# Kernel optimization log

Hardware: AMD Instinct MI355X
Metric: run time of the kernel (lower is better)

Reference implementation:

```python
import jax, jax.numpy as jnp
import numpy as np

N_NODES = 100000
N_EDGES = 3200000
STATE_DIM = 128
ACTION_DIM = 8


def _w(key, shape, scale=0.05):
    return (jax.random.normal(key, shape, dtype=jnp.float32) * scale)


def setup_inputs() -> dict:
    key = jax.random.key(0)
    ks = jax.random.split(key, 24)
    x = jax.random.normal(ks[0], (N_NODES, STATE_DIM), dtype=jnp.float32)
    edge_index = jax.random.randint(ks[1], (2, N_EDGES), 0, N_NODES, dtype=jnp.int64)
    inp = {
        "x": x,
        "edge_index": edge_index,
        # GCN layers (weights stored [in, out] so forward is x @ W + b)
        "W1": _w(ks[2], (STATE_DIM, 128)), "b1": jnp.zeros((128,), jnp.float32),
        "W2": _w(ks[3], (128, 128)),       "b2": jnp.zeros((128,), jnp.float32),
        "W3": _w(ks[4], (128, 64)),        "b3": jnp.zeros((64,), jnp.float32),
        # actor MLP 64->128->64->ACTION_DIM + softmax
        "Wa1": _w(ks[5], (64, 128)),  "ba1": jnp.zeros((128,), jnp.float32),
        "Wa2": _w(ks[6], (128, 64)),  "ba2": jnp.zeros((64,), jnp.float32),
        "Wa3": _w(ks[7], (64, ACTION_DIM)), "ba3": jnp.zeros((ACTION_DIM,), jnp.float32),
        # critic MLP 64->128->64->1
        "Wc1": _w(ks[8], (64, 128)),  "bc1": jnp.zeros((128,), jnp.float32),
        "Wc2": _w(ks[9], (128, 64)),  "bc2": jnp.zeros((64,), jnp.float32),
        "Wc3": _w(ks[10], (64, 1)),   "bc3": jnp.zeros((1,), jnp.float32),
    }
    return inp


def _gcn_conv(x, W, b, src, dst, norm):
    # GCNConv: D^{-1/2} (A + I) D^{-1/2} X W + b  (self loops already in src/dst)
    h = x @ W                                   # [N, out]
    msg = h[src] * norm[:, None]                # gather + per-edge scale
    agg = jax.ops.segment_sum(msg, dst, num_segments=N_NODES)
    return agg + b


def reference(x, edge_index,
              W1, b1, W2, b2, W3, b3,
              Wa1, ba1, Wa2, ba2, Wa3, ba3,
              Wc1, bc1, Wc2, bc2, Wc3, bc3):
    loop = jnp.arange(N_NODES, dtype=edge_index.dtype)
    src = jnp.concatenate([edge_index[0], loop])
    dst = jnp.concatenate([edge_index[1], loop])
    deg = jax.ops.segment_sum(jnp.ones_like(dst, dtype=x.dtype), dst,
                              num_segments=N_NODES)
    dinv = jax.lax.rsqrt(deg)                   # deg >= 1 via self loops
    norm = dinv[src] * dinv[dst]                # [E+N]

    # forward_gnn (dropout is identity in eval mode)
    h = jax.nn.relu(_gcn_conv(x, W1, b1, src, dst, norm))
    h = jax.nn.relu(_gcn_conv(h, W2, b2, src, dst, norm))
    h = _gcn_conv(h, W3, b3, src, dst, norm)    # [N, 64]

    a = jax.nn.relu(h @ Wa1 + ba1)
    a = jax.nn.relu(a @ Wa2 + ba2)
    probs = jax.nn.softmax(a @ Wa3 + ba3, axis=-1)   # [N, ACTION_DIM]

    c = jax.nn.relu(h @ Wc1 + bc1)
    c = jax.nn.relu(c @ Wc2 + bc2)
    values = c @ Wc3 + bc3                      # [N, 1]

    return jnp.concatenate([probs, values], axis=-1)  # [N, ACTION_DIM+1]
```

## Files before the change

kernel.cpp:

```cpp
#include <hip/hip_runtime.h>
#include <hip/hip_bf16.h>
#include <math.h>


#define WS_ALIGN(x) (((x) + 255) & ~(size_t)255)

constexpr int RNG  = 64;
constexpr int NRG  = 1563;
constexpr int NB   = 1024;
constexpr int CHK  = 16;

constexpr float S_FP8     = 64.0f;
constexpr float S_FP8_INV = 1.0f / 64.0f;

using bf16x8 = __attribute__((ext_vector_type(8))) short;
using f32x4  = __attribute__((ext_vector_type(4))) float;
using f32x2  = __attribute__((ext_vector_type(2))) float;

__device__ __forceinline__ float b2f(unsigned short u) {
    return __uint_as_float(((unsigned int)u) << 16);
}
__device__ __forceinline__ unsigned short f2b(float f) {
    __hip_bfloat16 hb = __float2bfloat16(f);
    return *(unsigned short*)&hb;
}
__device__ __forceinline__ unsigned char f2fp8(float f) {
    return (unsigned char)(__builtin_amdgcn_cvt_pk_fp8_f32(f, f, 0, false) & 0xff);
}
__device__ __forceinline__ int pad8(int v) { return (v + 7) & ~7; }

__device__ __forceinline__ void acc8(uint2 u, f32x2& a01, f32x2& a23,
                                     f32x2& a45, f32x2& a67) {
    a01 += __builtin_amdgcn_cvt_pk_f32_fp8((int)u.x, false);
    a23 += __builtin_amdgcn_cvt_pk_f32_fp8((int)u.x, true);
    a45 += __builtin_amdgcn_cvt_pk_f32_fp8((int)u.y, false);
    a67 += __builtin_amdgcn_cvt_pk_f32_fp8((int)u.y, true);
}


__global__ __launch_bounds__(256) void bucket_count_k(
    const int* __restrict__ dst, int* __restrict__ bcnt, int E,
    const float* __restrict__ W1, const float* __restrict__ W2,
    const float* __restrict__ W3, const float* __restrict__ Wa1,
    const float* __restrict__ Wc1, const float* __restrict__ Wa2,
    const float* __restrict__ Wc2,
    const float* __restrict__ b1, const float* __restrict__ b2,
    const float* __restrict__ b3,
    unsigned short* __restrict__ wt, float* __restrict__ bp) {
    __shared__ int c64[RNG];
    int b = blockIdx.x, t = threadIdx.x;

    int gi = b * 256 + t;
    if (gi < 73728) {
        const float* W; int off, K, OUT; int pm = 0;
        if (gi < 16384)      { W = W1;  off = 0;     K = 128; OUT = 128; }
        else if (gi < 32768) { W = W2;  off = 16384; K = 128; OUT = 128; pm = 1; }
        else if (gi < 40960) { W = W3;  off = 32768; K = 128; OUT = 64;  pm = 1; }
        else if (gi < 49152) { W = Wa1; off = 40960; K = 64;  OUT = 128; pm = 2; }
        else if (gi < 57344) { W = Wc1; off = 49152; K = 64;  OUT = 128; pm = 2; }
        else if (gi < 65536) { W = Wa2; off = 57344; K = 128; OUT = 64; }
        else                 { W = Wc2; off = 65536; K = 128; OUT = 64; }
        int j = gi - off, k = j / OUT, n = j - k * OUT;
        int kp = (pm == 1) ? ((k & 15) * 8 + (k >> 4))
               : (pm == 2) ? ((k & 15) * 4 + (k >> 4)) : k;
        wt[off + n * K + kp] = f2b(W[j]);
    } else if (gi < 74048) {
        int j = gi - 73728;
        if (j < 128)      bp[(j & 15) * 8 + (j >> 4)] = b1[j];
        else if (j < 256) { int j2 = j - 128; bp[128 + (j2 & 15) * 8 + (j2 >> 4)] = b2[j2]; }
        else              { int j3 = j - 256; bp[256 + (j3 & 15) * 4 + (j3 >> 4)] = b3[j3]; }
    }

    if (t < RNG) c64[t] = 0;
    __syncthreads();
    int ec = (E + NB - 1) / NB;
    int e0 = b * ec, e1 = min(E, e0 + ec);
    for (int e = e0 + t; e < e1; e += 256) {
        int d = __builtin_nontemporal_load(dst + e);
        atomicAdd(&c64[d / NRG], 1);
    }
    __syncthreads();
    if (t < RNG) bcnt[t * NB + b] = c64[t];
}

__global__ __launch_bounds__(256) void rsum_k(
    const int* __restrict__ bcnt, int* __restrict__ base, int* __restrict__ rtot) {
    __shared__ int s[256];
    int r = blockIdx.x, t = threadIdx.x;
    const int* row = bcnt + (size_t)r * NB;
    int v[4], loc = 0;
#pragma unroll
    for (int j = 0; j < 4; j++) { v[j] = row[t * 4 + j]; loc += v[j]; }
    s[t] = loc;
    __syncthreads();
    for (int d = 1; d < 256; d <<= 1) {
        int x = (t >= d) ? s[t - d] : 0;
        __syncthreads();
        s[t] += x;
        __syncthreads();
    }
    int run = s[t] - loc;
    int* bp2 = base + (size_t)r * NB + t * 4;
#pragma unroll
    for (int j = 0; j < 4; j++) { bp2[j] = run; run += v[j]; }
    if (t == 255) rtot[r] = s[255];
}

__global__ __launch_bounds__(256) void bucket_scatter_k(
    const int* __restrict__ src, const int* __restrict__ dst,
    const int* __restrict__ base, const int* __restrict__ rtot,
    unsigned* __restrict__ bucket, int E) {
    __shared__ int cur[RNG];
    __shared__ int rt[RNG];
    int b = blockIdx.x, t = threadIdx.x;
    if (t < RNG) rt[t] = rtot[t];
    __syncthreads();
    if (t < RNG) {
        int run = 0;
        for (int j = 0; j < t; j++) run += rt[j];
        cur[t] = run + base[(size_t)t * NB + b];
    }
    __syncthreads();
    int ec = (E + NB - 1) / NB;
    int e0 = b * ec, e1 = min(E, e0 + ec);
    for (int e = e0 + t; e < e1; e += 256) {
        int d = __builtin_nontemporal_load(dst + e);
        int sv = __builtin_nontemporal_load(src + e);
        int r = d / NRG;
        int pos = atomicAdd(&cur[r], 1);
        bucket[pos] = ((unsigned)(d - r * NRG) << 17) | (unsigned)sv;
    }
}

__global__ __launch_bounds__(256) void hist_bucket_k(
    const unsigned* __restrict__ bucket, const int* __restrict__ rtot,
    int* __restrict__ hist) {
    __shared__ int h[NRG];
    __shared__ int ss[2];
    int b = blockIdx.x, r = b & 63, c2 = b >> 6, t = threadIdx.x;
    for (int i = t; i < NRG; i += 256) h[i] = 0;
    if (t == 0) {
        int run = 0;
        for (int j = 0; j < r; j++) run += rtot[j];
        ss[0] = run; ss[1] = run + rtot[r];
    }
    __syncthreads();
    int s0 = ss[0], s1 = ss[1];
    int ec = (s1 - s0 + CHK - 1) / CHK;
    int e0 = s0 + c2 * ec, e1 = min(s1, e0 + ec);
    for (int e = e0 + t; e < e1; e += 256) {
        unsigned v = __builtin_nontemporal_load(bucket + e);
        atomicAdd(&h[v >> 17], 1);
    }
    __syncthreads();
    int* out = hist + ((size_t)r * CHK + c2) * NRG;
    for (int i = t; i < NRG; i += 256) out[i] = h[i];
}

__global__ __launch_bounds__(256) void sum_hist_dinv_k(
    const int* __restrict__ hist, int* __restrict__ cnt,
    float* __restrict__ dinv, int* __restrict__ bsum, int N) {
    __shared__ int sd[256];
    int t = threadIdx.x;
    int i = blockIdx.x * 256 + t;
    int s = 0;
    if (i < N) {
        int r = i / NRG, li = i - r * NRG;
        const int* hp = hist + ((size_t)r * CHK) * NRG + li;
#pragma unroll
        for (int c = 0; c < CHK; c++) s += hp[(size_t)c * NRG];
        cnt[i] = s;
        dinv[i] = rsqrtf((float)s + 1.0f);
    }
    sd[t] = (i < N) ? pad8(s) : 0;
    __syncthreads();
    for (int d = 128; d > 0; d >>= 1) {
        if (t < d) sd[t] += sd[t + d];
        __syncthreads();
    }
    if (t == 0) bsum[blockIdx.x] = sd[0];
}

__global__ void scan_off_pad_k(const int* __restrict__ cnt, const int* __restrict__ bsum,
                               int* __restrict__ rowptr, int* __restrict__ hist,
                               int* __restrict__ col, int N) {
    __shared__ int s[256];
    int t = threadIdx.x, b = blockIdx.x;

    int part = 0;
    for (int j = t; j < b; j += 256) part += bsum[j];
    s[t] = part;
    __syncthreads();
    for (int d = 128; d > 0; d >>= 1) {
        if (t < d) s[t] += s[t + d];
        __syncthreads();
    }
    int boffv = s[0];
    __syncthreads();

    int i = b * 256 + t;
    int cv = (i < N) ? cnt[i] : 0;
    int v = pad8(cv);
    if (i >= N) v = 0;
    s[t] = v;
    __syncthreads();
    for (int d = 1; d < 256; d <<= 1) {
        int x = (t >= d) ? s[t - d] : 0;
        __syncthreads();
        s[t] += x;
        __syncthreads();
    }
    if (b == (int)gridDim.x - 1 && t == 255) rowptr[N] = boffv + s[255];
    if (i < N) {
        int rp = s[t] - v + boffv;
        rowptr[i] = rp;
        int r = i / NRG, li = i - r * NRG;
        int* hp = hist + ((size_t)r * CHK) * NRG + li;
        int run = rp;
#pragma unroll
        for (int c = 0; c < CHK; c++) {
            int hv = hp[(size_t)c * NRG];
            hp[(size_t)c * NRG] = run;
            run += hv;
        }
        for (int e = rp + cv; e < rp + v; e++) col[e] = N;
    }
}

__global__ __launch_bounds__(256) void fill2_k(
    const unsigned* __restrict__ bucket, const int* __restrict__ rtot,
    const int* __restrict__ hist, int* __restrict__ col) {
    __shared__ int cur[NRG];
    __shared__ int ss[2];
    int b = blockIdx.x, r = b & 63, c2 = b >> 6, t = threadIdx.x;
    const int* hp = hist + ((size_t)r * CHK + c2) * NRG;
    for (int i = t; i < NRG; i += 256) cur[i] = hp[i];
    if (t == 0) {
        int run = 0;
        for (int j = 0; j < r; j++) run += rtot[j];
        ss[0] = run; ss[1] = run + rtot[r];
    }
    __syncthreads();
    int s0 = ss[0], s1 = ss[1];
    int ec = (s1 - s0 + CHK - 1) / CHK;
    int e0 = s0 + c2 * ec, e1 = min(s1, e0 + ec);
    for (int e = e0 + t; e < e1; e += 256) {
        unsigned v = __builtin_nontemporal_load(bucket + e);
        int slot = atomicAdd(&cur[v >> 17], 1);
        col[slot] = (int)(v & 0x1FFFFu);
    }
}


template <int K, int OUT, int EPI, bool AF32>
__global__ __launch_bounds__(256) void gemm2_k(
    const void* __restrict__ Xv, int ldx, const unsigned short* __restrict__ Wt,
    const float* __restrict__ sb, const float* __restrict__ w3b,
    const float* __restrict__ b3, void* __restrict__ Yv, int N, int NT) {
    constexpr int LDK = K + 8;
    __shared__ __align__(16) unsigned short Bs[OUT * LDK];
    __shared__ __align__(16) unsigned short As[64 * LDK];
    int t = threadIdx.x;

    for (int g = t; g < OUT * (K / 8); g += 256) {
        int r = g / (K / 8), q = g - r * (K / 8);
        *(uint4*)&Bs[r * LDK + q * 8] = *(const uint4*)(Wt + r * K + q * 8);
    }

    int wv = t >> 6, lane = t & 63;
    int lm = lane & 15, lq = lane >> 4;
    constexpr int CT = OUT / 16;

    for (int tile = blockIdx.x; tile < NT; tile += gridDim.x) {
        int rowBase = tile * 64;

        if constexpr (AF32) {
            const float* X = (const float*)Xv;
            for (int g = t; g < 64 * (K / 8); g += 256) {
                int r = g / (K / 8), q = g - r * (K / 8);
                int gr = rowBase + r;
                unsigned short us[8];
                if (gr < N) {
                    float4 v0 = *(const float4*)(X + (size_t)gr * ldx + q * 8);
                    float4 v1 = *(const float4*)(X + (size_t)gr * ldx + q * 8 + 4);
                    us[0] = f2b(v0.x); us[1] = f2b(v0.y); us[2] = f2b(v0.z); us[3] = f2b(v0.w);
                    us[4] = f2b(v1.x); us[5] = f2b(v1.y); us[6] = f2b(v1.z); us[7] = f2b(v1.w);
                } else {
#pragma unroll
                    for (int j = 0; j < 8; j++) us[j] = 0;
                }
                *(uint4*)&As[r * LDK + q * 8] = *(uint4*)us;
            }
        } else {
            const unsigned short* X = (const unsigned short*)Xv;
            for (int g = t; g < 64 * (K / 8); g += 256) {
                int r = g / (K / 8), q = g - r * (K / 8);
                int gr = rowBase + r;
                uint4 v = make_uint4(0, 0, 0, 0);
                if (gr < N) v = *(const uint4*)(X + (size_t)gr * ldx + q * 8);
                *(uint4*)&As[r * LDK + q * 8] = v;
            }
        }
        __syncthreads();

        f32x4 acc[CT];
#pragma unroll
        for (int c = 0; c < CT; c++) acc[c] = (f32x4){0.f, 0.f, 0.f, 0.f};

        const unsigned short* arow = &As[(wv * 16 + lm) * LDK + lq * 8];
#pragma unroll
        for (int kt = 0; kt < K / 32; kt++) {
            bf16x8 a = *(const bf16x8*)(arow + kt * 32);
#pragma unroll
            for (int c = 0; c < CT; c++) {
                bf16x8 b = *(const bf16x8*)&Bs[(c * 16 + lm) * LDK + kt * 32 + lq * 8];
                acc[c] = __builtin_amdgcn_mfma_f32_16x16x32_bf16(a, b, acc[c], 0, 0, 0);
            }
        }

        int r0 = rowBase + wv * 16 + lq * 4;
        if constexpr (EPI == 0) {
#pragma unroll
            for (int r = 0; r < 4; r++) {
                int gr = r0 + r;
                float scale = (gr < N) ? sb[gr] * S_FP8 : 0.f;
                if constexpr (OUT == 128) {
                    unsigned w0 = 0, w1 = 0;
                    w0 = __builtin_amdgcn_cvt_pk_fp8_f32(acc[0][r] * scale, acc[1][r] * scale, w0, false);
                    w0 = __builtin_amdgcn_cvt_pk_fp8_f32(acc[2][r] * scale, acc[3][r] * scale, w0, true);
                    w1 = __builtin_amdgcn_cvt_pk_fp8_f32(acc[4][r] * scale, acc[5][r] * scale, w1, false);
                    w1 = __builtin_amdgcn_cvt_pk_fp8_f32(acc[6][r] * scale, acc[7][r] * scale, w1, true);
                    *(uint2*)((unsigned char*)Yv + (size_t)gr * 128 + lm * 8) = make_uint2(w0, w1);
                } else {
                    unsigned w0 = 0;
                    w0 = __builtin_amdgcn_cvt_pk_fp8_f32(acc[0][r] * scale, acc[1][r] * scale, w0, false);
                    w0 = __builtin_amdgcn_cvt_pk_fp8_f32(acc[2][r] * scale, acc[3][r] * scale, w0, true);
                    *(unsigned*)((unsigned char*)Yv + (size_t)gr * 64 + lm * 4) = w0;
                }
            }
        }
        __syncthreads();
    }
}


template <bool RELU>
__global__ __launch_bounds__(256) void agg128_k(
    const unsigned char* __restrict__ H,
    const int* __restrict__ rowptr, const int* __restrict__ col,
    const float* __restrict__ dinv, const float* __restrict__ bias,
    unsigned short* __restrict__ Y, int N, int Ecap) {
    int tid = threadIdx.x;
    int node = blockIdx.x * 4 + (tid >> 6);
    if (node >= N) return;
    int lane = tid & 63;
    int grp = lane >> 4;
    int li8 = (lane & 15) * 8;

    f32x2 a01 = {0.f, 0.f}, a23 = {0.f, 0.f}, a45 = {0.f, 0.f}, a67 = {0.f, 0.f};
    if (grp == 0) {
        uint2 u = *(const uint2*)(H + (size_t)node * 128 + li8);
        acc8(u, a01, a23, a45, a67);
    }

    int start = rowptr[node], end = rowptr[node + 1];
    for (int e0 = start; e0 < end; e0 += 64) {
        int cv = col[min(e0 + lane, Ecap - 1)];
        int quads = min(64, end - e0) >> 2;
        for (int q = 0; q < quads; q += 2) {
            int s0 = __shfl(cv, 4 * q + grp, 64);
            int s1 = __shfl(cv, 4 * q + 4 + grp, 64);
            uint2 u0 = *(const uint2*)(H + (size_t)s0 * 128 + li8);
            uint2 u1 = *(const uint2*)(H + (size_t)s1 * 128 + li8);
            acc8(u0, a01, a23, a45, a67);
            acc8(u1, a01, a23, a45, a67);
        }
    }

#pragma unroll
    for (int w = 16; w < 64; w <<= 1) {
        a01[0] += __shfl_xor(a01[0], w, 64); a01[1] += __shfl_xor(a01[1], w, 64);
        a23[0] += __shfl_xor(a23[0], w, 64); a23[1] += __shfl_xor(a23[1], w, 64);
        a45[0] += __shfl_xor(a45[0], w, 64); a45[1] += __shfl_xor(a45[1], w, 64);
        a67[0] += __shfl_xor(a67[0], w, 64); a67[1] += __shfl_xor(a67[1], w, 64);
    }

    if (grp == 0) {
        float dv = dinv[node] * S_FP8_INV;
        float4 b0 = *(const float4*)(bias + li8);
        float4 b1 = *(const float4*)(bias + li8 + 4);
        float o0 = a01[0] * dv + b0.x, o1 = a01[1] * dv + b0.y;
        float o2 = a23[0] * dv + b0.z, o3 = a23[1] * dv + b0.w;
        float o4 = a45[0] * dv + b1.x, o5 = a45[1] * dv + b1.y;
        float o6 = a67[0] * dv + b1.z, o7 = a67[1] * dv + b1.w;
        if (RELU) {
            o0 = fmaxf(o0, 0.f); o1 = fmaxf(o1, 0.f); o2 = fmaxf(o2, 0.f); o3 = fmaxf(o3, 0.f);
            o4 = fmaxf(o4, 0.f); o5 = fmaxf(o5, 0.f); o6 = fmaxf(o6, 0.f); o7 = fmaxf(o7, 0.f);
        }
        unsigned short us[8] = {f2b(o0), f2b(o1), f2b(o2), f2b(o3),
                                f2b(o4), f2b(o5), f2b(o6), f2b(o7)};
        *(uint4*)(Y + (size_t)node * 128 + li8) = *(uint4*)us;
    }
}

__global__ __launch_bounds__(256) void agg64_k(
    const unsigned char* __restrict__ H,
    const int* __restrict__ rowptr, const int* __restrict__ col,
    const float* __restrict__ dinv, const float* __restrict__ bias,
    unsigned short* __restrict__ Y, int N, int Ecap) {
    int tid = threadIdx.x;
    int node = blockIdx.x * 4 + (tid >> 6);
    if (node >= N) return;
    int lane = tid & 63;
    int grp = lane >> 3;
    int li8 = (lane & 7) * 8;

    f32x2 a01 = {0.f, 0.f}, a23 = {0.f, 0.f}, a45 = {0.f, 0.f}, a67 = {0.f, 0.f};
    if (grp == 0) {
        uint2 u = *(const uint2*)(H + (size_t)node * 64 + li8);
        acc8(u, a01, a23, a45, a67);
    }

    int start = rowptr[node], end = rowptr[node + 1];
    for (int e0 = start; e0 < end; e0 += 64) {
        int cv = col[min(e0 + lane, Ecap - 1)];
        int octs = min(64, end - e0) >> 3;
        int o = 0;
        for (; o + 2 <= octs; o += 2) {
            int s0 = __shfl(cv, 8 * o + grp, 64);
            int s1 = __shfl(cv, 8 * o + 8 + grp, 64);
            uint2 u0 = *(const uint2*)(H + (size_t)s0 * 64 + li8);
            uint2 u1 = *(const uint2*)(H + (size_t)s1 * 64 + li8);
            acc8(u0, a01, a23, a45, a67);
            acc8(u1, a01, a23, a45, a67);
        }
        if (o < octs) {
            int s0 = __shfl(cv, 8 * o + grp, 64);
            uint2 u0 = *(const uint2*)(H + (size_t)s0 * 64 + li8);
            acc8(u0, a01, a23, a45, a67);
        }
    }

#pragma unroll
    for (int w = 8; w < 64; w <<= 1) {
        a01[0] += __shfl_xor(a01[0], w, 64); a01[1] += __shfl_xor(a01[1], w, 64);
        a23[0] += __shfl_xor(a23[0], w, 64); a23[1] += __shfl_xor(a23[1], w, 64);
        a45[0] += __shfl_xor(a45[0], w, 64); a45[1] += __shfl_xor(a45[1], w, 64);
        a67[0] += __shfl_xor(a67[0], w, 64); a67[1] += __shfl_xor(a67[1], w, 64);
    }

    if (grp == 0) {
        float dv = dinv[node] * S_FP8_INV;
        float4 b0 = *(const float4*)(bias + li8);
        float4 b1 = *(const float4*)(bias + li8 + 4);
        unsigned short us[8] = {
            f2b(a01[0] * dv + b0.x), f2b(a01[1] * dv + b0.y),
            f2b(a23[0] * dv + b0.z), f2b(a23[1] * dv + b0.w),
            f2b(a45[0] * dv + b1.x), f2b(a45[1] * dv + b1.y),
            f2b(a67[0] * dv + b1.z), f2b(a67[1] * dv + b1.w)};
        *(uint4*)(Y + (size_t)node * 64 + li8) = *(uint4*)us;
    }
}


__global__ __launch_bounds__(256) void headsB_k(
    const unsigned short* __restrict__ h3,
    const unsigned short* __restrict__ Wh1t,
    const float* __restrict__ ba1, const float* __restrict__ bc1,
    const unsigned short* __restrict__ Wa2t,
    const float* __restrict__ ba2,
    const unsigned short* __restrict__ Wc2t,
    const float* __restrict__ bc2,
    const float* __restrict__ Wa3, const float* __restrict__ ba3,
    const float* __restrict__ Wc3, const float* __restrict__ bc3,
    float* __restrict__ out, int N, int NT, int GH) {
    constexpr int LD64 = 72, LD128 = 136;
    __shared__ __align__(16) unsigned short Bs1[128 * LD64];
    __shared__ __align__(16) unsigned short Bs2[64 * LD128];
    __shared__ __align__(16) unsigned short As[4 * 16 * LD64];
    __shared__ __align__(16) unsigned short A1[4 * 16 * LD128];
    int t = threadIdx.x, wv = t >> 6, lane = t & 63;
    int lm = lane & 15, lq = lane >> 4;

    bool actor = (int)blockIdx.x < GH;
    const unsigned short* W1t = actor ? Wh1t : Wh1t + 128 * 64;
    const float* b1v = actor ? ba1 : bc1;
    const unsigned short* W2t = actor ? Wa2t : Wc2t;
    const float* b2v = actor ? ba2 : bc2;
    const float* w3  = actor ? Wa3 : Wc3;
    const float* b3v = actor ? ba3 : bc3;
    int tile0 = actor ? (int)blockIdx.x : (int)blockIdx.x - GH;

    for (int g = t; g < 128 * 8; g += 256) {
        int r = g >> 3, q = g & 7;
        *(uint4*)&Bs1[r * LD64 + q * 8] = *(const uint4*)(W1t + r * 64 + q * 8);
    }
    for (int g = t; g < 64 * 16; g += 256) {
        int r = g >> 4, q = g & 15;
        *(uint4*)&Bs2[r * LD128 + q * 8] = *(const uint4*)(W2t + r * 128 + q * 8);
    }
    __syncthreads();

    unsigned short* Asw = &As[wv * 16 * LD64];
    unsigned short* A1w = &A1[wv * 16 * LD128];

    for (int tile = tile0; tile < NT; tile += GH) {
        int rowBase = tile * 64 + wv * 16;

        for (int g = lane; g < 16 * 8; g += 64) {
            int r = g >> 3, q = g & 7;
            int gr = rowBase + r;
            uint4 v = make_uint4(0, 0, 0, 0);
            if (gr < N) v = *(const uint4*)(h3 + (size_t)gr * 64 + q * 8);
            *(uint4*)&Asw[r * LD64 + q * 8] = v;
        }

        f32x4 acc1[8];
#pragma unroll
        for (int c = 0; c < 8; c++) acc1[c] = (f32x4){0.f, 0.f, 0.f, 0.f};
        const unsigned short* arow = &Asw[lm * LD64 + lq * 8];
#pragma unroll
        for (int kt = 0; kt < 2; kt++) {
            bf16x8 a = *(const bf16x8*)(arow + kt * 32);
#pragma unroll
            for (int c = 0; c < 8; c++) {
                bf16x8 b = *(const bf16x8*)&Bs1[(c * 16 + lm) * LD64 + kt * 32 + lq * 8];
                acc1[c] = __builtin_amdgcn_mfma_f32_16x16x32_bf16(a, b, acc1[c], 0, 0, 0);
            }
        }
#pragma unroll
        for (int r = 0; r < 4; r++) {
            int lr = lq * 4 + r;
#pragma unroll
            for (int c = 0; c < 8; c++) {
                int colg = c * 16 + lm;
                float v = fmaxf(acc1[c][r] + b1v[colg], 0.f);
                A1w[lr * LD128 + colg] = f2b(v);
            }
        }

        f32x4 acc[4];
#pragma unroll
        for (int c = 0; c < 4; c++) acc[c] = (f32x4){0.f, 0.f, 0.f, 0.f};
        const unsigned short* arow2 = &A1w[lm * LD128 + lq * 8];
#pragma unroll
        for (int kt = 0; kt < 4; kt++) {
            bf16x8 a = *(const bf16x8*)(arow2 + kt * 32);
#pragma unroll
            for (int c = 0; c < 4; c++) {
                bf16x8 b = *(const bf16x8*)&Bs2[(c * 16 + lm) * LD128 + kt * 32 + lq * 8];
                acc[c] = __builtin_amdgcn_mfma_f32_16x16x32_bf16(a, b, acc[c], 0, 0, 0);
            }
        }

        int r0 = rowBase + lq * 4;
        if (actor) {
            float l[4][8];
#pragma unroll
            for (int r = 0; r < 4; r++)
#pragma unroll
                for (int a = 0; a < 8; a++) l[r][a] = 0.f;
#pragma unroll
            for (int c = 0; c < 4; c++) {
                int colg = c * 16 + lm;
#pragma unroll
                for (int r = 0; r < 4; r++) {
                    float v = fmaxf(acc[c][r] + b2v[colg], 0.f);
#pragma unroll
                    for (int a = 0; a < 8; a++)
                        l[r][a] = fmaf(v, w3[colg * 8 + a], l[r][a]);
                }
            }
#pragma unroll
            for (int w = 1; w < 16; w <<= 1)
#pragma unroll
                for (int r = 0; r < 4; r++)
#pragma unroll
                    for (int a = 0; a < 8; a++)
                        l[r][a] += __shfl_xor(l[r][a], w, 64);
            if (lm < 8) {
#pragma unroll
                for (int r = 0; r < 4; r++) {
                    int gr = r0 + r;
                    if (gr < N) {
                        float lg[8], m = -1e30f;
#pragma unroll
                        for (int a = 0; a < 8; a++) { lg[a] = l[r][a] + b3v[a]; m = fmaxf(m, lg[a]); }
                        float sum = 0.f;
#pragma unroll
                        for (int a = 0; a < 8; a++) { lg[a] = expf(lg[a] - m); sum += lg[a]; }
                        out[(size_t)gr * 9 + lm] = lg[lm] / sum;
                    }
                }
            }
        } else {
            float lv[4] = {0.f, 0.f, 0.f, 0.f};
#pragma unroll
            for (int c = 0; c < 4; c++) {
                int colg = c * 16 + lm;
#pragma unroll
                for (int r = 0; r < 4; r++) {
                    float v = fmaxf(acc[c][r] + b2v[colg], 0.f);
                    lv[r] = fmaf(v, w3[colg], lv[r]);
                }
            }
#pragma unroll
            for (int w = 1; w < 16; w <<= 1)
#pragma unroll
                for (int r = 0; r < 4; r++) lv[r] += __shfl_xor(lv[r], w, 64);
            if (lm == 0) {
#pragma unroll
                for (int r = 0; r < 4; r++) {
                    int gr = r0 + r;
                    if (gr < N) out[(size_t)gr * 9 + 8] = lv[r] + b3v[0];
                }
            }
        }
    }
}


extern "C" void kernel_launch(void* const* d_in, const int* in_sizes, int n_in,
                              void* d_out, int out_size, void* d_ws, size_t ws_size,
                              hipStream_t stream) {
    const float* x   = (const float*)d_in[0];
    const int*   ei  = (const int*)d_in[1];
    const float* W1  = (const float*)d_in[2];  const float* b1  = (const float*)d_in[3];
    const float* W2  = (const float*)d_in[4];  const float* b2  = (const float*)d_in[5];
    const float* W3  = (const float*)d_in[6];  const float* b3  = (const float*)d_in[7];
    const float* Wa1 = (const float*)d_in[8];  const float* ba1 = (const float*)d_in[9];
    const float* Wa2 = (const float*)d_in[10]; const float* ba2 = (const float*)d_in[11];
    const float* Wa3 = (const float*)d_in[12]; const float* ba3 = (const float*)d_in[13];
    const float* Wc1 = (const float*)d_in[14]; const float* bc1 = (const float*)d_in[15];
    const float* Wc2 = (const float*)d_in[16]; const float* bc2 = (const float*)d_in[17];
    const float* Wc3 = (const float*)d_in[18]; const float* bc3 = (const float*)d_in[19];
    float* out = (float*)d_out;

    const int N = in_sizes[0] / 128;
    const int E = in_sizes[1] / 2;
    const int* src = ei;
    const int* dst = ei + E;
    const int Ecap = E + 8 * N;
    const int Npad = ((N + 63) / 64) * 64;
    const int NT   = (N + 63) / 64;

    size_t off = 0;
    auto take = [&](size_t bytes) { size_t o = off; off = WS_ALIGN(off + bytes); return o; };
    char* ws = (char*)d_ws;
    unsigned short* h3     = (unsigned short*)(ws + take((size_t)N * 64 * 2));
    unsigned short* h      = (unsigned short*)(ws + take((size_t)N * 128 * 2));
    unsigned char*  hpr8   = (unsigned char*) (ws + take((size_t)(Npad + 64) * 128));
    int*            col    = (int*)(ws + take((size_t)Ecap * 4));
    unsigned short* wt     = (unsigned short*)(ws + take(73728 * 2));
    float* bperm  = (float*)(ws + take(320 * 4));
    float* dinv   = (float*)(ws + take((size_t)(N + 64) * 4));
    int*   cnt    = (int*)  (ws + take((size_t)N * 4));
    int*   rowptr = (int*)  (ws + take((size_t)(N + 1) * 4));
    int*   bcnt   = (int*)  (ws + take((size_t)RNG * NB * 4));
    int*   base   = (int*)  (ws + take((size_t)RNG * NB * 4));
    int*   rtot   = (int*)  (ws + take(RNG * 4));
    int*   bsum   = (int*)  (ws + take(512 * 4));
    unsigned* bucket = (unsigned*)h;
    int* hist = (int*)h3;
    (void)ws_size; (void)n_in; (void)out_size;

    const int nb  = (N + 255) / 256;
    const int GG128 = 768;
    const int GG64  = 1024;
    const int GH    = 512;

    const unsigned short* W1t  = wt;
    const unsigned short* W2t  = wt + 16384;
    const unsigned short* W3t  = wt + 32768;
    const unsigned short* Wh1t = wt + 40960;
    const unsigned short* Wa2t = wt + 57344;
    const unsigned short* Wc2t = wt + 65536;
    const float* b1p = bperm;
    const float* b2p = bperm + 128;
    const float* b3p = bperm + 256;

    bucket_count_k<<<NB, 256, 0, stream>>>(dst, bcnt, E,
                                           W1, W2, W3, Wa1, Wc1, Wa2, Wc2,
                                           b1, b2, b3, wt, bperm);
    rsum_k<<<RNG, 256, 0, stream>>>(bcnt, base, rtot);
    bucket_scatter_k<<<NB, 256, 0, stream>>>(src, dst, base, rtot, bucket, E);
    hist_bucket_k<<<RNG * CHK, 256, 0, stream>>>(bucket, rtot, hist);
    sum_hist_dinv_k<<<nb, 256, 0, stream>>>(hist, cnt, dinv, bsum, N);
    scan_off_pad_k<<<nb, 256, 0, stream>>>(cnt, bsum, rowptr, hist, col, N);
    fill2_k<<<RNG * CHK, 256, 0, stream>>>(bucket, rtot, hist, col);

    gemm2_k<128, 128, 0, true><<<GG128, 256, 0, stream>>>(
        x, 128, W1t, dinv, nullptr, nullptr, hpr8, N, NT);
    agg128_k<true><<<(N + 3) / 4, 256, 0, stream>>>(hpr8, rowptr, col, dinv, b1p, h, N, Ecap);
    gemm2_k<128, 128, 0, false><<<GG128, 256, 0, stream>>>(
        h, 128, W2t, dinv, nullptr, nullptr, hpr8, N, NT);
    agg128_k<true><<<(N + 3) / 4, 256, 0, stream>>>(hpr8, rowptr, col, dinv, b2p, h, N, Ecap);
    gemm2_k<128, 64, 0, false><<<GG64, 256, 0, stream>>>(
        h, 128, W3t, dinv, nullptr, nullptr, hpr8, N, NT);
    agg64_k<<<(N + 3) / 4, 256, 0, stream>>>(hpr8, rowptr, col, dinv, b3p, h3, N, Ecap);

    headsB_k<<<2 * GH, 256, 0, stream>>>(
        h3, Wh1t, ba1, bc1, Wa2t, ba2, Wc2t, bc2, Wa3, ba3, Wc3, bc3, out, N, NT, GH);
}
```

Measured before the change: 458.9 us.

## Fold histogram into bucket scatter and co-schedule CSR fill with first GEMM

The per-chunk destination histogram is now built with global atomics inside the bucket scatter kernel, which removes the separate hist_bucket pass over the bucket array. The hist buffer is zeroed in the first kernel. The CSR column fill and the layer-1 GEMM are merged into one launch, with blocks split 4:3 by block index, so these two independent tasks can overlap on the GPU. In exchange, 3.2M global atomics replace shared-memory atomics, and the fused kernel's shared footprint is sized for the GEMM, which may lower occupancy for the fill blocks.

```diff
diff --git a/kernel.cpp b/kernel.cpp
--- a/kernel.cpp
+++ b/kernel.cpp
@@ -9,6 +9,7 @@
 constexpr int NRG  = 1563;
 constexpr int NB   = 1024;
 constexpr int CHK  = 16;
+constexpr int HISTN = RNG * CHK * NRG;
 
 constexpr float S_FP8     = 64.0f;
 constexpr float S_FP8_INV = 1.0f / 64.0f;
@@ -46,7 +47,8 @@
     const float* __restrict__ Wc2,
     const float* __restrict__ b1, const float* __restrict__ b2,
     const float* __restrict__ b3,
-    unsigned short* __restrict__ wt, float* __restrict__ bp) {
+    unsigned short* __restrict__ wt, float* __restrict__ bp,
+    int* __restrict__ hist) {
     __shared__ int c64[RNG];
     int b = blockIdx.x, t = threadIdx.x;
 
@@ -71,6 +73,8 @@
         else              { int j3 = j - 256; bp[256 + (j3 & 15) * 4 + (j3 >> 4)] = b3[j3]; }
     }
 
+    for (int i2 = gi; i2 < HISTN; i2 += NB * 256) hist[i2] = 0;
+
     if (t < RNG) c64[t] = 0;
     __syncthreads();
     int ec = (E + NB - 1) / NB;
@@ -109,8 +113,10 @@
 __global__ __launch_bounds__(256) void bucket_scatter_k(
     const int* __restrict__ src, const int* __restrict__ dst,
     const int* __restrict__ base, const int* __restrict__ rtot,
-    unsigned* __restrict__ bucket, int E) {
+    unsigned* __restrict__ bucket, int* __restrict__ hist, int E) {
     __shared__ int cur[RNG];
+    __shared__ int sstart[RNG];
+    __shared__ int ecs[RNG];
     __shared__ int rt[RNG];
     int b = blockIdx.x, t = threadIdx.x;
     if (t < RNG) rt[t] = rtot[t];
@@ -118,7 +124,9 @@
     if (t < RNG) {
         int run = 0;
         for (int j = 0; j < t; j++) run += rt[j];
+        sstart[t] = run;
         cur[t] = run + base[(size_t)t * NB + b];
+        ecs[t] = (rt[t] + CHK - 1) / CHK;
     }
     __syncthreads();
     int ec = (E + NB - 1) / NB;
@@ -126,35 +134,12 @@
     for (int e = e0 + t; e < e1; e += 256) {
         int d = __builtin_nontemporal_load(dst + e);
         int sv = __builtin_nontemporal_load(src + e);
-        int r = d / NRG;
+        int r = d / NRG, li = d - r * NRG;
         int pos = atomicAdd(&cur[r], 1);
-        bucket[pos] = ((unsigned)(d - r * NRG) << 17) | (unsigned)sv;
-    }
-}
-
-__global__ __launch_bounds__(256) void hist_bucket_k(
-    const unsigned* __restrict__ bucket, const int* __restrict__ rtot,
-    int* __restrict__ hist) {
-    __shared__ int h[NRG];
-    __shared__ int ss[2];
-    int b = blockIdx.x, r = b & 63, c2 = b >> 6, t = threadIdx.x;
-    for (int i = t; i < NRG; i += 256) h[i] = 0;
-    if (t == 0) {
-        int run = 0;
-        for (int j = 0; j < r; j++) run += rtot[j];
-        ss[0] = run; ss[1] = run + rtot[r];
-    }
-    __syncthreads();
-    int s0 = ss[0], s1 = ss[1];
-    int ec = (s1 - s0 + CHK - 1) / CHK;
-    int e0 = s0 + c2 * ec, e1 = min(s1, e0 + ec);
-    for (int e = e0 + t; e < e1; e += 256) {
-        unsigned v = __builtin_nontemporal_load(bucket + e);
-        atomicAdd(&h[v >> 17], 1);
-    }
-    __syncthreads();
-    int* out = hist + ((size_t)r * CHK + c2) * NRG;
-    for (int i = t; i < NRG; i += 256) out[i] = h[i];
+        bucket[pos] = ((unsigned)li << 17) | (unsigned)sv;
+        int c2 = (int)((unsigned)(pos - sstart[r]) / (unsigned)ecs[r]);
+        atomicAdd(&hist[((size_t)r * CHK + c2) * NRG + li], 1);
+    }
 }
 
 __global__ __launch_bounds__(256) void sum_hist_dinv_k(
@@ -227,27 +212,97 @@
     }
 }
 
-__global__ __launch_bounds__(256) void fill2_k(
+
+__global__ __launch_bounds__(256) void fill2_gemm1_k(
     const unsigned* __restrict__ bucket, const int* __restrict__ rtot,
-    const int* __restrict__ hist, int* __restrict__ col) {
-    __shared__ int cur[NRG];
-    __shared__ int ss[2];
-    int b = blockIdx.x, r = b & 63, c2 = b >> 6, t = threadIdx.x;
-    const int* hp = hist + ((size_t)r * CHK + c2) * NRG;
-    for (int i = t; i < NRG; i += 256) cur[i] = hp[i];
-    if (t == 0) {
-        int run = 0;
-        for (int j = 0; j < r; j++) run += rtot[j];
-        ss[0] = run; ss[1] = run + rtot[r];
-    }
-    __syncthreads();
-    int s0 = ss[0], s1 = ss[1];
-    int ec = (s1 - s0 + CHK - 1) / CHK;
-    int e0 = s0 + c2 * ec, e1 = min(s1, e0 + ec);
-    for (int e = e0 + t; e < e1; e += 256) {
-        unsigned v = __builtin_nontemporal_load(bucket + e);
-        int slot = atomicAdd(&cur[v >> 17], 1);
-        col[slot] = (int)(v & 0x1FFFFu);
+    const int* __restrict__ hist, int* __restrict__ col,
+    const float* __restrict__ X, const unsigned short* __restrict__ Wt,
+    const float* __restrict__ dinv, unsigned char* __restrict__ Y,
+    int N, int NT) {
+    constexpr int LDK = 136;
+    __shared__ __align__(16) unsigned char smem[(128 * LDK + 64 * LDK) * 2];
+    int bid = blockIdx.x, t = threadIdx.x;
+    int sel = bid % 7;
+
+    if (sel < 4) {
+        int b = (bid / 7) * 4 + sel;
+        int* cur = (int*)smem;
+        int* ss  = (int*)(smem + NRG * 4);
+        int r = b & 63, c2 = b >> 6;
+        const int* hp = hist + ((size_t)r * CHK + c2) * NRG;
+        for (int i = t; i < NRG; i += 256) cur[i] = hp[i];
+        if (t == 0) {
+            int run = 0;
+            for (int j = 0; j < r; j++) run += rtot[j];
+            ss[0] = run; ss[1] = run + rtot[r];
+        }
+        __syncthreads();
+        int s0 = ss[0], s1 = ss[1];
+        int ec = (s1 - s0 + CHK - 1) / CHK;
+        int e0 = s0 + c2 * ec, e1 = min(s1, e0 + ec);
+        for (int e = e0 + t; e < e1; e += 256) {
+            unsigned v = __builtin_nontemporal_load(bucket + e);
+            int slot = atomicAdd(&cur[v >> 17], 1);
+            col[slot] = (int)(v & 0x1FFFFu);
+        }
+    } else {
+        int gb = (bid / 7) * 3 + (sel - 4);
+        unsigned short* Bs = (unsigned short*)smem;
+        unsigned short* As = (unsigned short*)(smem + 128 * LDK * 2);
+        for (int g = t; g < 128 * 16; g += 256) {
+            int r = g >> 4, q = g & 15;
+            *(uint4*)&Bs[r * LDK + q * 8] = *(const uint4*)(Wt + r * 128 + q * 8);
+        }
+        int wv = t >> 6, lane = t & 63;
+        int lm = lane & 15, lq = lane >> 4;
+
+        for (int tile = gb; tile < NT; tile += 768) {
+            int rowBase = tile * 64;
+            for (int g = t; g < 64 * 16; g += 256) {
+                int r = g >> 4, q = g & 15;
+                int gr = rowBase + r;
+                unsigned short us[8];
+                if (gr < N) {
+                    float4 v0 = *(const float4*)(X + (size_t)gr * 128 + q * 8);
+                    float4 v1 = *(const float4*)(X + (size_t)gr * 128 + q * 8 + 4);
+                    us[0] = f2b(v0.x); us[1] = f2b(v0.y); us[2] = f2b(v0.z); us[3] = f2b(v0.w);
+                    us[4] = f2b(v1.x); us[5] = f2b(v1.y); us[6] = f2b(v1.z); us[7] = f2b(v1.w);
+                } else {
+#pragma unroll
+                    for (int j = 0; j < 8; j++) us[j] = 0;
+                }
+                *(uint4*)&As[r * LDK + q * 8] = *(uint4*)us;
+            }
+            __syncthreads();
+
+            f32x4 acc[8];
+#pragma unroll
+            for (int c = 0; c < 8; c++) acc[c] = (f32x4){0.f, 0.f, 0.f, 0.f};
+            const unsigned short* arow = &As[(wv * 16 + lm) * LDK + lq * 8];
+#pragma unroll
+            for (int kt = 0; kt < 4; kt++) {
+                bf16x8 a = *(const bf16x8*)(arow + kt * 32);
+#pragma unroll
+                for (int c = 0; c < 8; c++) {
+                    bf16x8 bfrag = *(const bf16x8*)&Bs[(c * 16 + lm) * LDK + kt * 32 + lq * 8];
+                    acc[c] = __builtin_amdgcn_mfma_f32_16x16x32_bf16(a, bfrag, acc[c], 0, 0, 0);
+                }
+            }
+
+            int r0 = rowBase + wv * 16 + lq * 4;
+#pragma unroll
+            for (int r = 0; r < 4; r++) {
+                int gr = r0 + r;
+                float scale = (gr < N) ? dinv[gr] * S_FP8 : 0.f;
+                unsigned w0 = 0, w1 = 0;
+                w0 = __builtin_amdgcn_cvt_pk_fp8_f32(acc[0][r] * scale, acc[1][r] * scale, w0, false);
+                w0 = __builtin_amdgcn_cvt_pk_fp8_f32(acc[2][r] * scale, acc[3][r] * scale, w0, true);
+                w1 = __builtin_amdgcn_cvt_pk_fp8_f32(acc[4][r] * scale, acc[5][r] * scale, w1, false);
+                w1 = __builtin_amdgcn_cvt_pk_fp8_f32(acc[6][r] * scale, acc[7][r] * scale, w1, true);
+                *(uint2*)(Y + (size_t)gr * 128 + lm * 8) = make_uint2(w0, w1);
+            }
+            __syncthreads();
+        }
     }
 }
 
@@ -681,16 +736,15 @@
 
     bucket_count_k<<<NB, 256, 0, stream>>>(dst, bcnt, E,
                                            W1, W2, W3, Wa1, Wc1, Wa2, Wc2,
-                                           b1, b2, b3, wt, bperm);
+                                           b1, b2, b3, wt, bperm, hist);
     rsum_k<<<RNG, 256, 0, stream>>>(bcnt, base, rtot);
-    bucket_scatter_k<<<NB, 256, 0, stream>>>(src, dst, base, rtot, bucket, E);
-    hist_bucket_k<<<RNG * CHK, 256, 0, stream>>>(bucket, rtot, hist);
+    bucket_scatter_k<<<NB, 256, 0, stream>>>(src, dst, base, rtot, bucket, hist, E);
     sum_hist_dinv_k<<<nb, 256, 0, stream>>>(hist, cnt, dinv, bsum, N);
     scan_off_pad_k<<<nb, 256, 0, stream>>>(cnt, bsum, rowptr, hist, col, N);
-    fill2_k<<<RNG * CHK, 256, 0, stream>>>(bucket, rtot, hist, col);
-
-    gemm2_k<128, 128, 0, true><<<GG128, 256, 0, stream>>>(
-        x, 128, W1t, dinv, nullptr, nullptr, hpr8, N, NT);
+
+    fill2_gemm1_k<<<1792, 256, 0, stream>>>(bucket, rtot, hist, col,
+                                            x, W1t, dinv, hpr8, N, NT);
+
     agg128_k<true><<<(N + 3) / 4, 256, 0, stream>>>(hpr8, rowptr, col, dinv, b1p, h, N, Ecap);
     gemm2_k<128, 128, 0, false><<<GG128, 256, 0, stream>>>(
         h, 128, W2t, dinv, nullptr, nullptr, hpr8, N, NT);
```

After: 561.4 us. 1.22x slower.
